# Performance work log

Hardware: AMD Instinct MI355X
Metric: run time of the kernel (lower is better)

## Reference

```python
import jax, jax.numpy as jnp
import numpy as np

NQ = 10          # qubits
NT = 32          # tokens (LCU terms)
DM = 512         # d_model
DEG = 2          # qsvt degree
B = 128          # batch
NPQC = 4 * NQ    # params per PQC application
DIM = 2 ** NQ    # statevector dimension


def ansatz14_spec(q, layers=1):
    spec = []
    for _ in range(layers):
        spec += [('ry', (i,)) for i in range(q)]
        spec += [('crx', (i, (i + 1) % q)) for i in range(q - 1, -1, -1)]
        spec += [('ry', (i,)) for i in range(q)]
        spec += [('crx', (i, (i - 1) % q)) for i in [q - 1] + list(range(q - 1))]
    return spec

SPEC = ansatz14_spec(NQ, 1)


def _gate_ry(theta):
    h = theta * 0.5
    c = jnp.cos(h)
    s = jnp.sin(h)
    m = jnp.stack([jnp.stack([c, -s], -1), jnp.stack([s, c], -1)], -2)
    return m.astype(jnp.complex64)  # (N,2,2)


def _gate_rx(theta):
    h = theta * 0.5
    c = jnp.cos(h).astype(jnp.complex64)
    s = (-1j) * jnp.sin(h).astype(jnp.complex64)
    return jnp.stack([jnp.stack([c, s], -1), jnp.stack([s, c], -1)], -2)


def _apply_1q(state, mats, wire, q):
    # state: (N, 2^q) complex; mats: (N,2,2); wire 0 is most significant bit
    N = state.shape[0]
    a = 2 ** wire
    bdim = 2 ** (q - wire - 1)
    s = state.reshape(N, a, 2, bdim)
    return jnp.einsum('nij,najb->naib', mats, s).reshape(N, 2 ** q)


def _apply_crx(state, theta, c, t, q):
    # controlled-RX: control wire c, target wire t
    N = state.shape[0]
    st = state.reshape((N,) + (2,) * q)
    ax = 1 + c
    s0 = jnp.take(st, 0, axis=ax)   # control = 0 branch: untouched
    s1 = jnp.take(st, 1, axis=ax)   # control = 1 branch: apply RX on target
    tp = t if t < c else t - 1      # target wire position after removing control axis
    s1n = _apply_1q(s1.reshape(N, -1), _gate_rx(theta), tp, q - 1).reshape(s1.shape)
    return jnp.stack([s0, s1n], axis=ax).reshape(N, 2 ** q)


def _apply_pqc(state, params, q):
    # params: (N, NPQC); fixed small gate list -> Python loop is fine
    for k, (fn, w) in enumerate(SPEC):
        th = params[:, k]
        if fn == 'ry':
            state = _apply_1q(state, _gate_ry(th), w[0], q)
        else:
            state = _apply_crx(state, th, w[0], w[1], q)
    return state


def _apply_lcu(states, params, lcu):
    # states: (B, DIM) complex; params: (B, L, NPQC); lcu: (B, L) complex
    Bn, L = lcu.shape
    rep = jnp.repeat(states, L, axis=0)                    # (B*L, DIM)
    st = _apply_pqc(rep, params.reshape(Bn * L, NPQC), NQ)
    return jnp.einsum('bld,bl->bd', st.reshape(Bn, L, DIM), lcu)


def _measure_xyz(state, q):
    # Pauli expectations per wire: order [X_0..X_{q-1}, Y_0.., Z_0..]
    N = state.shape[0]
    xs, ys, zs = [], [], []
    for w in range(q):
        s = state.reshape(N, 2 ** w, 2, -1)
        a0, a1 = s[:, :, 0, :], s[:, :, 1, :]
        cross = jnp.sum(jnp.conj(a0) * a1, axis=(1, 2))
        xs.append(2.0 * jnp.real(cross))
        ys.append(2.0 * jnp.imag(cross))
        zs.append(jnp.sum(jnp.abs(a0) ** 2 - jnp.abs(a1) ** 2, axis=(1, 2)))
    return jnp.stack(xs + ys + zs, axis=1).astype(jnp.float32)  # (B, 3q)


def reference(tokens_emb, W, b, lcu_re, lcu_im, qsvt_coeffs, ff_params):
    Bn, L, D = tokens_emb.shape
    L = min(L, NT)
    pqc_params = tokens_emb[:, :L] @ W.T + b               # (B, L, NPQC)
    lcu = (lcu_re + 1j * lcu_im).astype(jnp.complex64)[:L]
    lcu = lcu / jnp.sum(jnp.abs(lcu))
    lcu_b = jnp.broadcast_to(lcu[None], (Bn, L))
    init = jnp.zeros((Bn, DIM), jnp.complex64).at[:, 0].set(1.0)
    acc = qsvt_coeffs[0].astype(jnp.complex64) * init
    mono = init
    for k in range(1, DEG + 1):
        mono = _apply_lcu(mono, pqc_params, lcu_b)
        acc = acc + qsvt_coeffs[k].astype(jnp.complex64) * mono
    state = acc / jnp.sum(jnp.abs(qsvt_coeffs))
    state = state / jnp.linalg.norm(state, axis=-1, keepdims=True)
    ffp = jnp.broadcast_to(ff_params[None], (Bn, NPQC))
    state = _apply_pqc(state, ffp, NQ)
    return _measure_xyz(state, NQ)


def setup_inputs():
    key = jax.random.key(0)
    ks = jax.random.split(key, 7)
    return {
        'tokens_emb': jax.random.normal(ks[0], (B, NT, DM), jnp.float32),
        'W': jax.random.normal(ks[1], (NPQC, DM), jnp.float32) * 0.05,
        'b': jax.random.normal(ks[2], (NPQC,), jnp.float32),
        'lcu_re': jax.random.normal(ks[3], (NT,), jnp.float32),
        'lcu_im': jax.random.normal(ks[4], (NT,), jnp.float32),
        'qsvt_coeffs': jax.random.normal(ks[5], (DEG + 1,), jnp.float32),
        'ff_params': jax.random.normal(ks[6], (NPQC,), jnp.float32),
    }
```

## Files before the change

kernel.cpp:

```cpp
#include <hip/hip_runtime.h>
#include <hip/hip_bf16.h>


#define NQ   10
#define NT   32
#define DM   512
#define BATCH 128
#define NPQC 40
#define DIM  1024
#define NROWS (BATCH * NT)
#define PSTRIDE (BATCH * DIM)

typedef float v2f __attribute__((ext_vector_type(2)));

__device__ __forceinline__ v2f Jrot(v2f v) {
  return __builtin_shufflevector(v, -v, 1, 2);
}
__device__ __forceinline__ v2f Jc(v2f v) {
  return __builtin_shufflevector(-v, v, 1, 2);
}


template<int B>
__device__ __forceinline__ void g_ry(v2f (&a)[16], float c, float s) {
  static_assert(B >= 6, "RY targets must be register bits");
  constexpr int m = 1 << (B - 6);
#pragma unroll
  for (int r = 0; r < 16; ++r) {
    if (!(r & m)) {
      int r1 = r | m;
      v2f a0 = a[r], a1 = a[r1];
      a[r]  = c * a0 - s * a1;
      a[r1] = s * a0 + c * a1;
    }
  }
}

template<int BC, int BT>
__device__ __forceinline__ void g_crx(v2f (&a)[16], int lane, float c, float s) {
  static_assert(BT >= 6, "CRX targets must be register bits");
  constexpr int m = 1 << (BT - 6);
  bool lane_ok = (BC >= 6) || ((lane >> BC) & 1);
  float ce = lane_ok ? c : 1.f;
  float se = lane_ok ? s : 0.f;
#pragma unroll
  for (int r = 0; r < 16; ++r) {
    if (!(r & m)) {
      if constexpr (BC >= 6) { if (!((r >> (BC - 6)) & 1)) continue; }
      int r1 = r | m;
      v2f a0 = a[r], a1 = a[r1];
      a[r]  = ce * a0 + se * Jrot(a1);
      a[r1] = ce * a1 + se * Jrot(a0);
    }
  }
}

template<int L0, int L1, int L2, int L3>
__device__ __forceinline__ void remap(v2f (&a)[16], v2f* __restrict__ slab,
                                      int lane) {
  constexpr int LM = (1 << L0) | (1 << L1) | (1 << L2) | (1 << L3);
#pragma unroll
  for (int r = 0; r < 16; ++r) {
    int f = 0;
    if (L0 < 4 && (r & 1)) f |= 1 << L0;
    if (L1 < 4 && (r & 2)) f |= 1 << L1;
    if (L2 < 4 && (r & 4)) f |= 1 << L2;
    if (L3 < 4 && (r & 8)) f |= 1 << L3;
    slab[r * 64 + (lane ^ f)] = a[r];
  }
  asm volatile("s_waitcnt lgkmcnt(0)" ::: "memory");
  int la = lane & ~LM & 63;
  la |= ((lane >> L0) & 1) << 6;
  la |= ((lane >> L1) & 1) << 7;
  la |= ((lane >> L2) & 1) << 8;
  la |= ((lane >> L3) & 1) << 9;
  if (L0 < 4) la |= ((lane >> L0) & 1) << L0;
  if (L1 < 4) la |= ((lane >> L1) & 1) << L1;
  if (L2 < 4) la |= ((lane >> L2) & 1) << L2;
  if (L3 < 4) la |= ((lane >> L3) & 1) << L3;
#pragma unroll
  for (int r = 0; r < 16; ++r) {
    int rc = ((r & 1) ? (1 << L0) : 0) | ((r & 2) ? (1 << L1) : 0)
           | ((r & 4) ? (1 << L2) : 0) | ((r & 8) ? (1 << L3) : 0);
    a[r] = slab[la ^ rc];
  }
}

template<bool SKIP_HEAD>
__device__ __forceinline__ void apply_pqc_phased(v2f (&a)[16],
    const float2* __restrict__ cs, v2f* __restrict__ slab, int lane) {
  float2 t;
#define RYB(k, B)      t = cs[k]; g_ry<B>(a, t.x, t.y);
#define CXB(k, BC, BT) t = cs[k]; g_crx<BC, BT>(a, lane, t.x, t.y);
  if constexpr (!SKIP_HEAD) {
    RYB(0,9) RYB(1,8) RYB(2,7) RYB(3,6)
    remap<5,4,3,2>(a, slab, lane);
    RYB(4,6) RYB(5,7) RYB(6,8) RYB(7,9)
    remap<1,0,2,3>(a, slab, lane);
    RYB(8,6) RYB(9,7)
  }
  CXB(10,7,8) CXB(11,6,7) CXB(12,3,6)
  remap<1,0,2,3>(a, slab, lane);
  CXB(13,8,9) CXB(14,7,8) CXB(15,6,7) CXB(16,5,6)
  remap<2,3,4,5>(a, slab, lane);
  CXB(17,8,9) CXB(18,7,8) CXB(19,6,7)
  RYB(20,6) RYB(21,7) RYB(22,8) RYB(23,9)
  remap<2,3,4,5>(a, slab, lane);
  RYB(24,6) RYB(25,7) RYB(26,8) RYB(27,9)
  remap<1,0,2,3>(a, slab, lane);
  RYB(28,6) RYB(29,7)
  CXB(30,7,6) CXB(31,8,7) CXB(32,9,8) CXB(33,4,9)
  remap<4,5,1,0>(a, slab, lane);
  CXB(34,7,6) CXB(35,8,7) CXB(36,9,8) CXB(37,2,9)
  remap<2,3,4,5>(a, slab, lane);
  CXB(38,7,6) CXB(39,8,7)
#undef RYB
#undef CXB
}

__device__ __forceinline__ int p8_lane_canon(int lane) {
  return (((lane >> 1) & 1) << 9) | ((lane & 1) << 8) | (((lane >> 2) & 1) << 7)
       | (((lane >> 3) & 1) << 6) | (((lane >> 4) & 1) << 5) | (((lane >> 5) & 1) << 4);
}

__global__ __launch_bounds__(256) void params_kernel(
    const float* __restrict__ emb, const float* __restrict__ W,
    const float* __restrict__ bias,
    const float* __restrict__ lcu_re, const float* __restrict__ lcu_im,
    const float* __restrict__ ffp,
    float2* __restrict__ cs, float2* __restrict__ ffcs, float2* __restrict__ lcu) {
  int blk = blockIdx.x;
  int tid = threadIdx.x;
  if (blk == 256) {
    if (tid < NPQC) {
      float h = 0.5f * ffp[tid];
      ffcs[tid] = make_float2(cosf(h), sinf(h));
    }
    if (tid == 64) {
      float ssum = 0.f;
      for (int i = 0; i < NT; ++i) {
        float re = lcu_re[i], im = lcu_im[i];
        ssum += sqrtf(re * re + im * im);
      }
      float inv = 1.f / ssum;
      for (int i = 0; i < NT; ++i)
        lcu[i] = make_float2(lcu_re[i] * inv, lcu_im[i] * inv);
    }
    return;
  }

  __shared__ float Asl[16 * 516];
  int row0 = blk * 16;

  const float4* eg = (const float4*)(emb + (size_t)row0 * DM);
#pragma unroll
  for (int i = 0; i < 8; ++i) {
    int e = tid + i * 256;
    int r = e >> 7, k4 = e & 127;
    float4 v = eg[e];
    *(float4*)&Asl[r * 516 + k4 * 4] = v;
  }
  __syncthreads();

  int kq = tid >> 6;
  int lane = tid & 63;
  int rg = lane >> 3;
  int cg = lane & 7;

  const float* Ar0 = &Asl[(2 * rg) * 516 + kq * 128];
  const float* Ar1 = Ar0 + 516;
  const float* Bg  = W + (size_t)(5 * cg) * DM + kq * 128;

  float acc[2][5] = {};
#pragma unroll 4
  for (int k = 0; k < 128; k += 4) {
    float4 a0 = *(const float4*)(Ar0 + k);
    float4 a1 = *(const float4*)(Ar1 + k);
#pragma unroll
    for (int j = 0; j < 5; ++j) {
      float4 b = *(const float4*)(Bg + j * DM + k);
      acc[0][j] += a0.x * b.x + a0.y * b.y + a0.z * b.z + a0.w * b.w;
      acc[1][j] += a1.x * b.x + a1.y * b.y + a1.z * b.z + a1.w * b.w;
    }
  }

  __syncthreads();
  float* red = Asl;
#pragma unroll
  for (int i = 0; i < 2; ++i)
#pragma unroll
    for (int j = 0; j < 5; ++j)
      red[kq * 644 + (2 * rg + i) * 40 + 5 * cg + j] = acc[i][j];
  __syncthreads();

  for (int o = tid; o < 640; o += 256) {
    float v = bias[o % 40] + red[o] + red[644 + o] + red[1288 + o] + red[1932 + o];
    float h = 0.5f * v;
    cs[(size_t)blk * 640 + o] = make_float2(cosf(h), sinf(h));
  }
}

template<bool FIRST>
__global__ __launch_bounds__(256) void pqc_step(
    const float2* __restrict__ cs, const float2* __restrict__ lcu,
    const v2f* __restrict__ src, v2f* __restrict__ dst) {
  __shared__ v2f slabs[4][1024];
  int lane = threadIdx.x & 63;
  int wvu = __builtin_amdgcn_readfirstlane(threadIdx.x >> 6);
  int blk = blockIdx.x;
  int b = blk >> 3, qq = blk & 7;
  int l = qq * 4 + wvu;
  const float2* csrow = cs + (size_t)(b * NT + l) * NPQC;
  v2f* slab = slabs[wvu];

  v2f a[16];
  if constexpr (FIRST) {
    float2 f5 = csrow[5], f4 = csrow[4], f6 = csrow[6], f7 = csrow[7];
    float2 f2 = csrow[2], f3 = csrow[3];
    float2 f8 = csrow[8], f9 = csrow[9], f0 = csrow[0], f1 = csrow[1];
    float lp = ((lane & 1) ? f5.y : f5.x);
    lp *= ((lane & 2) ? f4.y : f4.x);
    lp *= ((lane & 4) ? f6.y : f6.x);
    lp *= ((lane & 8) ? f7.y : f7.x);
    lp *= ((lane & 16) ? f2.y : f2.x);
    lp *= ((lane & 32) ? f3.y : f3.x);
#pragma unroll
    for (int r = 0; r < 16; ++r) {
      float rp = ((r & 1) ? f8.y : f8.x) * ((r & 2) ? f9.y : f9.x)
               * ((r & 4) ? f0.y : f0.x) * ((r & 8) ? f1.y : f1.x);
      a[r].x = lp * rp;
      a[r].y = 0.f;
    }
  } else {
    const v2f* s = src + (size_t)b * DIM;
#pragma unroll
    for (int r = 0; r < 16; ++r) {
      int n = r * 64 + lane;
      v2f acc = (v2f)(0.f);
#pragma unroll
      for (int q = 0; q < 8; ++q) acc += s[n + q * PSTRIDE];
      a[r] = acc;
    }
  }

  apply_pqc_phased<FIRST>(a, csrow, slab, lane);

  float2 w = lcu[l];
  int pl = p8_lane_canon(lane);
  pl ^= (pl >> 5);
#pragma unroll
  for (int r = 0; r < 16; ++r) {
    int rc = ((r & 1) << 3) | ((r & 2) << 1) | ((r & 4) >> 1) | ((r & 8) >> 3);
    slab[pl ^ rc] = w.x * a[r] + w.y * Jc(a[r]);
  }
  __syncthreads();

  v2f* dst_b = dst + (size_t)(qq * BATCH + b) * DIM;
#pragma unroll
  for (int i = 0; i < 4; ++i) {
    int n = threadIdx.x + i * 256;
    int ph = n ^ (n >> 5);
    v2f sum = (v2f)(0.f);
#pragma unroll
    for (int s = 0; s < 4; ++s) sum += slabs[s][ph];
    dst_b[n] = sum;
  }
}

__global__ __launch_bounds__(256) void final_kernel(
    const v2f* __restrict__ part1, const v2f* __restrict__ part2,
    const float* __restrict__ qsvt, const float2* __restrict__ ffcs,
    float* __restrict__ out) {
  __shared__ v2f slabs[4][1024];
  int lane = threadIdx.x & 63;
  int wvu = __builtin_amdgcn_readfirstlane(threadIdx.x >> 6);
  int b = blockIdx.x * 4 + wvu;
  float q0 = qsvt[0], q1 = qsvt[1], q2 = qsvt[2];

  v2f a[16];
  const v2f* p1 = part1 + (size_t)b * DIM;
  const v2f* p2 = part2 + (size_t)b * DIM;
#pragma unroll
  for (int r = 0; r < 16; ++r) {
    int n = r * 64 + lane;
    v2f m1 = (v2f)(0.f), m2 = (v2f)(0.f);
#pragma unroll
    for (int q = 0; q < 8; ++q) {
      m1 += p1[n + q * PSTRIDE];
      m2 += p2[n + q * PSTRIDE];
    }
    a[r] = q1 * m1 + q2 * m2;
  }
  if (lane == 0) a[0].x += q0;

  float nn = 0.f;
#pragma unroll
  for (int r = 0; r < 16; ++r) nn += a[r].x * a[r].x + a[r].y * a[r].y;
#pragma unroll
  for (int o = 1; o < 64; o <<= 1) nn += __shfl_xor(nn, o);
  float inv = 1.f / sqrtf(nn);
#pragma unroll
  for (int r = 0; r < 16; ++r) a[r] *= inv;

  apply_pqc_phased<false>(a, ffcs, slabs[wvu], lane);

  constexpr int BPOS[10] = {1, 0, 2, 3, 4, 5, 6, 7, 8, 9};
#pragma unroll
  for (int w = 0; w < NQ; ++w) {
    const int p = BPOS[w];
    float xr = 0.f, xi = 0.f, zz = 0.f;
    if (p >= 6) {
      const int m = 1 << (p - 6);
#pragma unroll
      for (int r = 0; r < 16; ++r) {
        float mag = a[r].x * a[r].x + a[r].y * a[r].y;
        zz += (r & m) ? -mag : mag;
        if (!(r & m)) {
          int r1 = r | m;
          xr += a[r].x * a[r1].x + a[r].y * a[r1].y;
          xi += a[r].x * a[r1].y - a[r].y * a[r1].x;
        }
      }
    } else {
      const int lm = 1 << p;
      bool lo = !(lane & lm);
#pragma unroll
      for (int r = 0; r < 16; ++r) {
        float mag = a[r].x * a[r].x + a[r].y * a[r].y;
        zz += lo ? mag : -mag;
        float pr = __shfl_xor(a[r].x, lm);
        float pi = __shfl_xor(a[r].y, lm);
        if (lo) {
          xr += a[r].x * pr + a[r].y * pi;
          xi += a[r].x * pi - a[r].y * pr;
        }
      }
    }
#pragma unroll
    for (int o = 1; o < 64; o <<= 1) {
      xr += __shfl_xor(xr, o);
      xi += __shfl_xor(xi, o);
      zz += __shfl_xor(zz, o);
    }
    if (lane == 0) {
      out[b * 30 + w]      = 2.f * xr;
      out[b * 30 + 10 + w] = 2.f * xi;
      out[b * 30 + 20 + w] = zz;
    }
  }
}


extern "C" void kernel_launch(void* const* d_in, const int* in_sizes, int n_in,
                              void* d_out, int out_size, void* d_ws, size_t ws_size,
                              hipStream_t stream) {
  const float* emb    = (const float*)d_in[0];
  const float* W      = (const float*)d_in[1];
  const float* bias   = (const float*)d_in[2];
  const float* lcu_re = (const float*)d_in[3];
  const float* lcu_im = (const float*)d_in[4];
  const float* qsvt   = (const float*)d_in[5];
  const float* ffp    = (const float*)d_in[6];
  float* out = (float*)d_out;

  char* ws = (char*)d_ws;
  float2* cs    = (float2*)ws;
  float2* ffcs  = (float2*)(ws + 1310720);
  float2* lcu   = (float2*)(ws + 1311040);
  v2f*    part1 = (v2f*)(ws + 1311744);
  v2f*    part2 = (v2f*)(ws + 1311744 + 8388608);

  params_kernel<<<257, 256, 0, stream>>>(emb, W, bias, lcu_re, lcu_im, ffp,
                                         cs, ffcs, lcu);
  pqc_step<true><<<1024, 256, 0, stream>>>(cs, lcu, nullptr, part1);
  pqc_step<false><<<1024, 256, 0, stream>>>(cs, lcu, part1, part2);
  final_kernel<<<BATCH / 4, 256, 0, stream>>>(part1, part2, qsvt, ffcs, out);
}
```

Baseline: 158.7 us.

## Process two LCU terms per wave with interleaved LDS remaps

```diff
diff --git a/kernel.cpp b/kernel.cpp
--- a/kernel.cpp
+++ b/kernel.cpp
@@ -13,6 +13,8 @@
 
 typedef float v2f __attribute__((ext_vector_type(2)));
 
+#define WAITLDS asm volatile("s_waitcnt lgkmcnt(0)" ::: "memory")
+
 __device__ __forceinline__ v2f Jrot(v2f v) {
   return __builtin_shufflevector(v, -v, 1, 2);
 }
@@ -56,9 +58,8 @@
 }
 
 template<int L0, int L1, int L2, int L3>
-__device__ __forceinline__ void remap(v2f (&a)[16], v2f* __restrict__ slab,
-                                      int lane) {
-  constexpr int LM = (1 << L0) | (1 << L1) | (1 << L2) | (1 << L3);
+__device__ __forceinline__ void remap_w(const v2f (&a)[16],
+                                        v2f* __restrict__ slab, int lane) {
 #pragma unroll
   for (int r = 0; r < 16; ++r) {
     int f = 0;
@@ -68,7 +69,12 @@
     if (L3 < 4 && (r & 8)) f |= 1 << L3;
     slab[r * 64 + (lane ^ f)] = a[r];
   }
-  asm volatile("s_waitcnt lgkmcnt(0)" ::: "memory");
+}
+
+template<int L0, int L1, int L2, int L3>
+__device__ __forceinline__ void remap_r(v2f (&a)[16],
+                                        const v2f* __restrict__ slab, int lane) {
+  constexpr int LM = (1 << L0) | (1 << L1) | (1 << L2) | (1 << L3);
   int la = lane & ~LM & 63;
   la |= ((lane >> L0) & 1) << 6;
   la |= ((lane >> L1) & 1) << 7;
@@ -86,41 +92,136 @@
   }
 }
 
+template<int L0, int L1, int L2, int L3>
+__device__ __forceinline__ void remap(v2f (&a)[16], v2f* __restrict__ slab,
+                                      int lane) {
+  remap_w<L0, L1, L2, L3>(a, slab, lane);
+  WAITLDS;
+  remap_r<L0, L1, L2, L3>(a, slab, lane);
+}
+
+template<int I> struct RL;
+template<> struct RL<0> { static constexpr int A=5,B=4,C=3,D=2; };
+template<> struct RL<1> { static constexpr int A=1,B=0,C=2,D=3; };
+template<> struct RL<2> { static constexpr int A=1,B=0,C=2,D=3; };
+template<> struct RL<3> { static constexpr int A=2,B=3,C=4,D=5; };
+template<> struct RL<4> { static constexpr int A=2,B=3,C=4,D=5; };
+template<> struct RL<5> { static constexpr int A=1,B=0,C=2,D=3; };
+template<> struct RL<6> { static constexpr int A=4,B=5,C=1,D=0; };
+template<> struct RL<7> { static constexpr int A=2,B=3,C=4,D=5; };
+
+template<int I>
+__device__ __forceinline__ void rmw(const v2f (&a)[16], v2f* __restrict__ slab,
+                                    int lane) {
+  remap_w<RL<I>::A, RL<I>::B, RL<I>::C, RL<I>::D>(a, slab, lane);
+}
+template<int I>
+__device__ __forceinline__ void rmr(v2f (&a)[16], const v2f* __restrict__ slab,
+                                    int lane) {
+  remap_r<RL<I>::A, RL<I>::B, RL<I>::C, RL<I>::D>(a, slab, lane);
+}
+
+template<int PH, bool SKIP_HEAD>
+__device__ __forceinline__ void phase_gates(v2f (&a)[16],
+    const float2* __restrict__ cs, int lane) {
+  float2 t;
+#define RYk(B_, k)      t = cs[k]; g_ry<B_>(a, t.x, t.y);
+#define CXk(BC, BT, k)  t = cs[k]; g_crx<BC, BT>(a, lane, t.x, t.y);
+  if constexpr (PH == 0) { RYk(9,0) RYk(8,1) RYk(7,2) RYk(6,3) }
+  else if constexpr (PH == 1) { RYk(6,4) RYk(7,5) RYk(8,6) RYk(9,7) }
+  else if constexpr (PH == 2) {
+    if constexpr (!SKIP_HEAD) { RYk(6,8) RYk(7,9) }
+    CXk(7,8,10) CXk(6,7,11) CXk(3,6,12)
+  }
+  else if constexpr (PH == 3) { CXk(8,9,13) CXk(7,8,14) CXk(6,7,15) CXk(5,6,16) }
+  else if constexpr (PH == 4) { CXk(8,9,17) CXk(7,8,18) CXk(6,7,19)
+                                RYk(6,20) RYk(7,21) RYk(8,22) RYk(9,23) }
+  else if constexpr (PH == 5) { RYk(6,24) RYk(7,25) RYk(8,26) RYk(9,27) }
+  else if constexpr (PH == 6) { RYk(6,28) RYk(7,29)
+                                CXk(7,6,30) CXk(8,7,31) CXk(9,8,32) CXk(4,9,33) }
+  else if constexpr (PH == 7) { CXk(7,6,34) CXk(8,7,35) CXk(9,8,36) CXk(2,9,37) }
+  else { CXk(7,6,38) CXk(8,7,39) }
+#undef RYk
+#undef CXk
+}
+
 template<bool SKIP_HEAD>
-__device__ __forceinline__ void apply_pqc_phased(v2f (&a)[16],
+__device__ __forceinline__ void apply_pqc_dual(v2f (&A)[16], v2f (&B)[16],
+    const float2* __restrict__ csA, const float2* __restrict__ csB,
+    v2f* __restrict__ slab, int lane) {
+#define STEP_PAIR(i, ip1) \
+  phase_gates<ip1, SKIP_HEAD>(A, csA, lane); \
+  WAITLDS; rmr<i>(B, slab, lane); rmw<ip1>(A, slab, lane); \
+  phase_gates<ip1, SKIP_HEAD>(B, csB, lane); \
+  WAITLDS; rmr<ip1>(A, slab, lane); rmw<ip1>(B, slab, lane);
+  if constexpr (!SKIP_HEAD) {
+    phase_gates<0, false>(A, csA, lane);
+    rmw<0>(A, slab, lane);
+    phase_gates<0, false>(B, csB, lane);
+    WAITLDS; rmr<0>(A, slab, lane); rmw<0>(B, slab, lane);
+    STEP_PAIR(0, 1)
+    STEP_PAIR(1, 2)
+  } else {
+    phase_gates<2, true>(A, csA, lane);
+    rmw<2>(A, slab, lane);
+    phase_gates<2, true>(B, csB, lane);
+    WAITLDS; rmr<2>(A, slab, lane); rmw<2>(B, slab, lane);
+  }
+  STEP_PAIR(2, 3)
+  STEP_PAIR(3, 4)
+  STEP_PAIR(4, 5)
+  STEP_PAIR(5, 6)
+  STEP_PAIR(6, 7)
+  phase_gates<8, SKIP_HEAD>(A, csA, lane);
+  WAITLDS; rmr<7>(B, slab, lane);
+  phase_gates<8, SKIP_HEAD>(B, csB, lane);
+#undef STEP_PAIR
+}
+
+__device__ __forceinline__ void apply_pqc_single(v2f (&a)[16],
     const float2* __restrict__ cs, v2f* __restrict__ slab, int lane) {
-  float2 t;
-#define RYB(k, B)      t = cs[k]; g_ry<B>(a, t.x, t.y);
-#define CXB(k, BC, BT) t = cs[k]; g_crx<BC, BT>(a, lane, t.x, t.y);
-  if constexpr (!SKIP_HEAD) {
-    RYB(0,9) RYB(1,8) RYB(2,7) RYB(3,6)
-    remap<5,4,3,2>(a, slab, lane);
-    RYB(4,6) RYB(5,7) RYB(6,8) RYB(7,9)
-    remap<1,0,2,3>(a, slab, lane);
-    RYB(8,6) RYB(9,7)
-  }
-  CXB(10,7,8) CXB(11,6,7) CXB(12,3,6)
-  remap<1,0,2,3>(a, slab, lane);
-  CXB(13,8,9) CXB(14,7,8) CXB(15,6,7) CXB(16,5,6)
-  remap<2,3,4,5>(a, slab, lane);
-  CXB(17,8,9) CXB(18,7,8) CXB(19,6,7)
-  RYB(20,6) RYB(21,7) RYB(22,8) RYB(23,9)
-  remap<2,3,4,5>(a, slab, lane);
-  RYB(24,6) RYB(25,7) RYB(26,8) RYB(27,9)
-  remap<1,0,2,3>(a, slab, lane);
-  RYB(28,6) RYB(29,7)
-  CXB(30,7,6) CXB(31,8,7) CXB(32,9,8) CXB(33,4,9)
-  remap<4,5,1,0>(a, slab, lane);
-  CXB(34,7,6) CXB(35,8,7) CXB(36,9,8) CXB(37,2,9)
-  remap<2,3,4,5>(a, slab, lane);
-  CXB(38,7,6) CXB(39,8,7)
-#undef RYB
-#undef CXB
+  phase_gates<0, false>(a, cs, lane);
+  remap<RL<0>::A, RL<0>::B, RL<0>::C, RL<0>::D>(a, slab, lane);
+  phase_gates<1, false>(a, cs, lane);
+  remap<RL<1>::A, RL<1>::B, RL<1>::C, RL<1>::D>(a, slab, lane);
+  phase_gates<2, false>(a, cs, lane);
+  remap<RL<2>::A, RL<2>::B, RL<2>::C, RL<2>::D>(a, slab, lane);
+  phase_gates<3, false>(a, cs, lane);
+  remap<RL<3>::A, RL<3>::B, RL<3>::C, RL<3>::D>(a, slab, lane);
+  phase_gates<4, false>(a, cs, lane);
+  remap<RL<4>::A, RL<4>::B, RL<4>::C, RL<4>::D>(a, slab, lane);
+  phase_gates<5, false>(a, cs, lane);
+  remap<RL<5>::A, RL<5>::B, RL<5>::C, RL<5>::D>(a, slab, lane);
+  phase_gates<6, false>(a, cs, lane);
+  remap<RL<6>::A, RL<6>::B, RL<6>::C, RL<6>::D>(a, slab, lane);
+  phase_gates<7, false>(a, cs, lane);
+  remap<RL<7>::A, RL<7>::B, RL<7>::C, RL<7>::D>(a, slab, lane);
+  phase_gates<8, false>(a, cs, lane);
 }
 
 __device__ __forceinline__ int p8_lane_canon(int lane) {
   return (((lane >> 1) & 1) << 9) | ((lane & 1) << 8) | (((lane >> 2) & 1) << 7)
        | (((lane >> 3) & 1) << 6) | (((lane >> 4) & 1) << 5) | (((lane >> 5) & 1) << 4);
+}
+
+__device__ __forceinline__ void product_init(v2f (&a)[16],
+    const float2* __restrict__ csrow, int lane) {
+  float2 f5 = csrow[5], f4 = csrow[4], f6 = csrow[6], f7 = csrow[7];
+  float2 f2 = csrow[2], f3 = csrow[3];
+  float2 f8 = csrow[8], f9 = csrow[9], f0 = csrow[0], f1 = csrow[1];
+  float lp = ((lane & 1) ? f5.y : f5.x);
+  lp *= ((lane & 2) ? f4.y : f4.x);
+  lp *= ((lane & 4) ? f6.y : f6.x);
+  lp *= ((lane & 8) ? f7.y : f7.x);
+  lp *= ((lane & 16) ? f2.y : f2.x);
+  lp *= ((lane & 32) ? f3.y : f3.x);
+#pragma unroll
+  for (int r = 0; r < 16; ++r) {
+    float rp = ((r & 1) ? f8.y : f8.x) * ((r & 2) ? f9.y : f9.x)
+             * ((r & 4) ? f0.y : f0.x) * ((r & 8) ? f1.y : f1.x);
+    a[r].x = lp * rp;
+    a[r].y = 0.f;
+  }
 }
 
 __global__ __launch_bounds__(256) void params_kernel(
@@ -208,50 +309,37 @@
   int lane = threadIdx.x & 63;
   int wvu = __builtin_amdgcn_readfirstlane(threadIdx.x >> 6);
   int blk = blockIdx.x;
-  int b = blk >> 3, qq = blk & 7;
-  int l = qq * 4 + wvu;
-  const float2* csrow = cs + (size_t)(b * NT + l) * NPQC;
+  int b = blk >> 2, qq = blk & 3;
+  int l0 = qq * 8 + wvu * 2;
+  const float2* csA = cs + (size_t)(b * NT + l0) * NPQC;
+  const float2* csB = csA + NPQC;
   v2f* slab = slabs[wvu];
 
-  v2f a[16];
+  v2f A[16], B[16];
   if constexpr (FIRST) {
-    float2 f5 = csrow[5], f4 = csrow[4], f6 = csrow[6], f7 = csrow[7];
-    float2 f2 = csrow[2], f3 = csrow[3];
-    float2 f8 = csrow[8], f9 = csrow[9], f0 = csrow[0], f1 = csrow[1];
-    float lp = ((lane & 1) ? f5.y : f5.x);
-    lp *= ((lane & 2) ? f4.y : f4.x);
-    lp *= ((lane & 4) ? f6.y : f6.x);
-    lp *= ((lane & 8) ? f7.y : f7.x);
-    lp *= ((lane & 16) ? f2.y : f2.x);
-    lp *= ((lane & 32) ? f3.y : f3.x);
-#pragma unroll
-    for (int r = 0; r < 16; ++r) {
-      float rp = ((r & 1) ? f8.y : f8.x) * ((r & 2) ? f9.y : f9.x)
-               * ((r & 4) ? f0.y : f0.x) * ((r & 8) ? f1.y : f1.x);
-      a[r].x = lp * rp;
-      a[r].y = 0.f;
-    }
+    product_init(A, csA, lane);
+    product_init(B, csB, lane);
   } else {
     const v2f* s = src + (size_t)b * DIM;
 #pragma unroll
     for (int r = 0; r < 16; ++r) {
       int n = r * 64 + lane;
-      v2f acc = (v2f)(0.f);
-#pragma unroll
-      for (int q = 0; q < 8; ++q) acc += s[n + q * PSTRIDE];
-      a[r] = acc;
-    }
-  }
-
-  apply_pqc_phased<FIRST>(a, csrow, slab, lane);
-
-  float2 w = lcu[l];
+      v2f acc = s[n] + s[n + PSTRIDE] + s[n + 2 * PSTRIDE] + s[n + 3 * PSTRIDE];
+      A[r] = acc;
+      B[r] = acc;
+    }
+  }
+
+  apply_pqc_dual<FIRST>(A, B, csA, csB, slab, lane);
+
+  float2 wA = lcu[l0], wB = lcu[l0 + 1];
   int pl = p8_lane_canon(lane);
   pl ^= (pl >> 5);
 #pragma unroll
   for (int r = 0; r < 16; ++r) {
     int rc = ((r & 1) << 3) | ((r & 2) << 1) | ((r & 4) >> 1) | ((r & 8) >> 3);
-    slab[pl ^ rc] = w.x * a[r] + w.y * Jc(a[r]);
+    slab[pl ^ rc] = wA.x * A[r] + wA.y * Jc(A[r])
+                  + wB.x * B[r] + wB.y * Jc(B[r]);
   }
   __syncthreads();
 
@@ -260,9 +348,7 @@
   for (int i = 0; i < 4; ++i) {
     int n = threadIdx.x + i * 256;
     int ph = n ^ (n >> 5);
-    v2f sum = (v2f)(0.f);
-#pragma unroll
-    for (int s = 0; s < 4; ++s) sum += slabs[s][ph];
+    v2f sum = slabs[0][ph] + slabs[1][ph] + slabs[2][ph] + slabs[3][ph];
     dst_b[n] = sum;
   }
 }
@@ -285,7 +371,7 @@
     int n = r * 64 + lane;
     v2f m1 = (v2f)(0.f), m2 = (v2f)(0.f);
 #pragma unroll
-    for (int q = 0; q < 8; ++q) {
+    for (int q = 0; q < 4; ++q) {
       m1 += p1[n + q * PSTRIDE];
       m2 += p2[n + q * PSTRIDE];
     }
@@ -302,9 +388,10 @@
 #pragma unroll
   for (int r = 0; r < 16; ++r) a[r] *= inv;
 
-  apply_pqc_phased<false>(a, ffcs, slabs[wvu], lane);
+  apply_pqc_single(a, ffcs, slabs[wvu], lane);
 
   constexpr int BPOS[10] = {1, 0, 2, 3, 4, 5, 6, 7, 8, 9};
+  float prt[30];
 #pragma unroll
   for (int w = 0; w < NQ; ++w) {
     const int p = BPOS[w];
@@ -336,17 +423,21 @@
         }
       }
     }
-#pragma unroll
-    for (int o = 1; o < 64; o <<= 1) {
-      xr += __shfl_xor(xr, o);
-      xi += __shfl_xor(xi, o);
-      zz += __shfl_xor(zz, o);
-    }
-    if (lane == 0) {
-      out[b * 30 + w]      = 2.f * xr;
-      out[b * 30 + 10 + w] = 2.f * xi;
-      out[b * 30 + 20 + w] = zz;
-    }
+    prt[w]      = xr;
+    prt[10 + w] = xi;
+    prt[20 + w] = zz;
+  }
+
+  float* tb = (float*)slabs[wvu];
+#pragma unroll
+  for (int v = 0; v < 30; ++v) tb[v * 65 + lane] = prt[v];
+  WAITLDS;
+  if (lane < 30) {
+    float s = 0.f;
+#pragma unroll
+    for (int k = 0; k < 64; ++k) s += tb[lane * 65 + k];
+    float sc = (lane < 20) ? 2.f : 1.f;
+    out[b * 30 + lane] = sc * s;
   }
 }
 
@@ -368,11 +459,11 @@
   float2* ffcs  = (float2*)(ws + 1310720);
   float2* lcu   = (float2*)(ws + 1311040);
   v2f*    part1 = (v2f*)(ws + 1311744);
-  v2f*    part2 = (v2f*)(ws + 1311744 + 8388608);
+  v2f*    part2 = (v2f*)(ws + 1311744 + 4194304);
 
   params_kernel<<<257, 256, 0, stream>>>(emb, W, bias, lcu_re, lcu_im, ffp,
                                          cs, ffcs, lcu);
-  pqc_step<true><<<1024, 256, 0, stream>>>(cs, lcu, nullptr, part1);
-  pqc_step<false><<<1024, 256, 0, stream>>>(cs, lcu, part1, part2);
+  pqc_step<true><<<512, 256, 0, stream>>>(cs, lcu, nullptr, part1);
+  pqc_step<false><<<512, 256, 0, stream>>>(cs, lcu, part1, part2);
   final_kernel<<<BATCH / 4, 256, 0, stream>>>(part1, part2, qsvt, ffcs, out);
 }
```

Measured after the change: 233.8 us. 1.47x slower.
